# Performance work log

Measured on AMD Instinct MI355X. Metric: run time of the kernel, lower is better.

## Reference

```python
import jax, jax.numpy as jnp
import numpy as np

D_MODEL = 1024
N_HEADS = 16
HEAD_DIM = D_MODEL // N_HEADS
B, S = 4, 2048


def setup_inputs() -> dict:
    key = jax.random.key(0)
    ks = jax.random.split(key, 11)
    scale = 1.0 / np.sqrt(D_MODEL)
    inp = {
        "query": jax.random.normal(ks[0], (B, S, D_MODEL), jnp.float32),
        "key": jax.random.normal(ks[1], (B, S, D_MODEL), jnp.float32),
        "value": jax.random.normal(ks[2], (B, S, D_MODEL), jnp.float32),
        "Wq": jax.random.normal(ks[3], (D_MODEL, D_MODEL), jnp.float32) * scale,
        "bq": jnp.zeros((D_MODEL,), jnp.float32),
        "Wk": jax.random.normal(ks[4], (D_MODEL, D_MODEL), jnp.float32) * scale,
        "bk": jnp.zeros((D_MODEL,), jnp.float32),
        "Wv": jax.random.normal(ks[5], (D_MODEL, D_MODEL), jnp.float32) * scale,
        "bv": jnp.zeros((D_MODEL,), jnp.float32),
        "Wo": jax.random.normal(ks[6], (D_MODEL, D_MODEL), jnp.float32) * scale,
        "bo": jnp.zeros((D_MODEL,), jnp.float32),
    }
    return inp


def _split_heads(x):
    b, s, _ = x.shape
    return x.reshape(b, s, N_HEADS, HEAD_DIM).transpose(0, 2, 1, 3)  # b h s d


def reference(query, key, value, Wq, bq, Wk, bk, Wv, bv, Wo, bo):
    Q = _split_heads(query @ Wq.T + bq)
    K = _split_heads(key @ Wk.T + bk)
    V = _split_heads(value @ Wv.T + bv)
    scale = 1.0 / jnp.sqrt(jnp.float32(HEAD_DIM))
    energy = jnp.einsum("bhqd,bhkd->bhqk", Q, K) * scale  # full N x N scores
    attn = jax.nn.softmax(energy, axis=-1)
    x = jnp.einsum("bhqk,bhkd->bhqd", attn, V)
    x = x.transpose(0, 2, 1, 3).reshape(query.shape[0], -1, D_MODEL)
    return x @ Wo.T + bo
```

## Files before the change

kernel.cpp:

```cpp
#include <hip/hip_runtime.h>
#include <cstdint>
#include <cstddef>


typedef unsigned short u16;
typedef unsigned u32;
typedef short short8 __attribute__((ext_vector_type(8)));
typedef __bf16 bf16x8 __attribute__((ext_vector_type(8)));
typedef float f32x4 __attribute__((ext_vector_type(4)));
typedef float f32x16 __attribute__((ext_vector_type(16)));
typedef unsigned short u16x4 __attribute__((ext_vector_type(4)));
typedef unsigned u32x2 __attribute__((ext_vector_type(2)));
typedef unsigned u32x4 __attribute__((ext_vector_type(4)));
typedef int iv2 __attribute__((ext_vector_type(2)));

__device__ __forceinline__ u16 f2bf(float f) {
  unsigned u = __builtin_bit_cast(unsigned, f);
  u += 0x7fffu + ((u >> 16) & 1u);
  return (u16)(u >> 16);
}
__device__ __forceinline__ bf16x8 bc8(short8 v) { return __builtin_bit_cast(bf16x8, v); }
__device__ __forceinline__ u32 pk_bf16(float a, float b) {
  u32 r;
  asm("v_cvt_pk_bf16_f32 %0, %1, %2" : "=v"(r) : "v"(a), "v"(b));
  return r;
}
__device__ __forceinline__ void gload16(const u16* g, u16* l) {
  __builtin_amdgcn_global_load_lds((const __attribute__((address_space(1))) void*)g,
                                   (__attribute__((address_space(3))) void*)l, 16, 0, 0);
}

__global__ __launch_bounds__(256) void cvt_all(const float* __restrict__ q,
                                               const float* __restrict__ k,
                                               const float* __restrict__ v,
                                               const float* __restrict__ wq,
                                               const float* __restrict__ wk,
                                               const float* __restrict__ wv,
                                               const float* __restrict__ wo,
                                               u16* __restrict__ xq, u16* __restrict__ xk,
                                               u16* __restrict__ xv, u16* __restrict__ wqb,
                                               u16* __restrict__ wkb, u16* __restrict__ wvb,
                                               u16* __restrict__ wob) {
  const size_t i4 = (size_t)blockIdx.x * 256 + threadIdx.x;
  const size_t A4 = 1ull << 21, W4 = 1ull << 18;
  const float* s;
  u16* d;
  size_t off;
  if (i4 < 3 * A4) {
    const int r = (int)(i4 >> 21);
    off = i4 & (A4 - 1);
    s = r == 0 ? q : (r == 1 ? k : v);
    d = r == 0 ? xq : (r == 1 ? xk : xv);
  } else {
    const size_t t = i4 - 3 * A4;
    const int r = (int)(t >> 18);
    off = t & (W4 - 1);
    s = r == 0 ? wq : (r == 1 ? wk : (r == 2 ? wv : wo));
    d = r == 0 ? wqb : (r == 1 ? wkb : (r == 2 ? wvb : wob));
  }
  const f32x4 a = ((const f32x4*)s)[off];
  u32x2 o = {pk_bf16(a[0], a[1]), pk_bf16(a[2], a[3])};
  ((u32x2*)d)[off] = o;
}

__device__ __forceinline__ bf16x8 ldf(const u16* buf, int row, int g) {
  return bc8(*(const short8*)(buf + row * 32 + g * 8));
}

__device__ __forceinline__ void gemm_core(u16* lds, const u16* __restrict__ A,
                                          const u16* __restrict__ Bw,
                                          const float* __restrict__ bias,
                                          void* __restrict__ C, int mode, float oscale) {
  const int t = threadIdx.x;
  const int w = t >> 6, l = t & 63, g = l >> 4, m = l & 15;
  const int wr = w >> 1, wc = w & 1;
  const int m0 = blockIdx.x * 128, n0 = blockIdx.y * 256;
  const u16* gA = A + (size_t)m0 * 1024;
  const u16* gB = Bw + (size_t)n0 * 1024;

  f32x4 acc[4][8];
  const f32x4 z = {0.f, 0.f, 0.f, 0.f};
#pragma unroll
  for (int i = 0; i < 4; ++i)
#pragma unroll
    for (int j = 0; j < 8; ++j) acc[i][j] = z;

#pragma unroll
  for (int tt = 0; tt < 2; ++tt) {
    u16* sA = lds + tt * 12288;
    u16* sB = sA + 4096;
    const int ko = tt * 32;
#pragma unroll
    for (int r = 0; r < 2; ++r) {
      const int c = r * 256 + t;
      gload16(gA + (size_t)(c >> 2) * 1024 + (c & 3) * 8 + ko, sA + c * 8);
    }
#pragma unroll
    for (int r = 0; r < 4; ++r) {
      const int c = r * 256 + t;
      gload16(gB + (size_t)(c >> 2) * 1024 + (c & 3) * 8 + ko, sB + c * 8);
    }
  }
  asm volatile("s_waitcnt vmcnt(6)" ::: "memory");
  __builtin_amdgcn_s_barrier();

  bf16x8 af[4], bfr[8];
  int cb = 0;
  for (int tt = 0; tt < 32; ++tt) {
    u16* bA = lds + cb * 12288;
    u16* bB = bA + 4096;
    const int sbi = (cb == 0) ? 2 : cb - 1;
    u16* sA = lds + sbi * 12288;
    u16* sB = sA + 4096;
    const int ko = (tt + 2) * 32;
    const bool st = tt < 30;

    af[0] = ldf(bA, wr * 64 + m, g);
    af[1] = ldf(bA, wr * 64 + 16 + m, g);
#pragma unroll
    for (int j = 0; j < 4; ++j) bfr[j] = ldf(bB, wc * 128 + j * 16 + m, g);
    if (st) {
#pragma unroll
      for (int r = 0; r < 2; ++r) {
        const int c = r * 256 + t;
        gload16(gA + (size_t)(c >> 2) * 1024 + (c & 3) * 8 + ko, sA + c * 8);
      }
    }
    __builtin_amdgcn_s_barrier();
    __builtin_amdgcn_s_setprio(1);
#pragma unroll
    for (int i = 0; i < 2; ++i)
#pragma unroll
      for (int j = 0; j < 4; ++j)
        acc[i][j] = __builtin_amdgcn_mfma_f32_16x16x32_bf16(af[i], bfr[j], acc[i][j], 0, 0, 0);
    __builtin_amdgcn_s_setprio(0);
    __builtin_amdgcn_s_barrier();

#pragma unroll
    for (int j = 4; j < 8; ++j) bfr[j] = ldf(bB, wc * 128 + j * 16 + m, g);
    if (st) {
#pragma unroll
      for (int r = 0; r < 2; ++r) {
        const int c = r * 256 + t;
        gload16(gB + (size_t)(c >> 2) * 1024 + (c & 3) * 8 + ko, sB + c * 8);
      }
    }
    __builtin_amdgcn_s_barrier();
    __builtin_amdgcn_s_setprio(1);
#pragma unroll
    for (int i = 0; i < 2; ++i)
#pragma unroll
      for (int j = 4; j < 8; ++j)
        acc[i][j] = __builtin_amdgcn_mfma_f32_16x16x32_bf16(af[i], bfr[j], acc[i][j], 0, 0, 0);
    __builtin_amdgcn_s_setprio(0);
    __builtin_amdgcn_s_barrier();

    af[2] = ldf(bA, wr * 64 + 32 + m, g);
    af[3] = ldf(bA, wr * 64 + 48 + m, g);
    if (st) {
#pragma unroll
      for (int r = 2; r < 4; ++r) {
        const int c = r * 256 + t;
        gload16(gB + (size_t)(c >> 2) * 1024 + (c & 3) * 8 + ko, sB + c * 8);
      }
    }
    __builtin_amdgcn_s_barrier();
    __builtin_amdgcn_s_setprio(1);
#pragma unroll
    for (int i = 2; i < 4; ++i)
#pragma unroll
      for (int j = 0; j < 4; ++j)
        acc[i][j] = __builtin_amdgcn_mfma_f32_16x16x32_bf16(af[i], bfr[j], acc[i][j], 0, 0, 0);
    __builtin_amdgcn_s_setprio(0);
    __builtin_amdgcn_s_barrier();

    __builtin_amdgcn_s_setprio(1);
#pragma unroll
    for (int i = 2; i < 4; ++i)
#pragma unroll
      for (int j = 4; j < 8; ++j)
        acc[i][j] = __builtin_amdgcn_mfma_f32_16x16x32_bf16(af[i], bfr[j], acc[i][j], 0, 0, 0);
    __builtin_amdgcn_s_setprio(0);
    if (tt < 30)
      asm volatile("s_waitcnt vmcnt(6)" ::: "memory");
    else
      asm volatile("s_waitcnt vmcnt(0)" ::: "memory");
    __builtin_amdgcn_s_barrier();
    cb = (cb == 2) ? 0 : cb + 1;
  }

  float bv[8];
#pragma unroll
  for (int j = 0; j < 8; ++j) bv[j] = bias[n0 + wc * 128 + j * 16 + m];

  if (mode == 2) {
#pragma unroll
    for (int i = 0; i < 4; ++i)
#pragma unroll
      for (int j = 0; j < 8; ++j) {
        const int row0 = m0 + wr * 64 + i * 16 + g * 4;
        const int col = n0 + wc * 128 + j * 16 + m;
        u16x4 o;
#pragma unroll
        for (int r = 0; r < 4; ++r) o[r] = f2bf((acc[i][j][r] + bv[j]) * oscale);
        *(u16x4*)((u16*)C + ((size_t)(row0 >> 11) * 1024 + col) * 2048 + (row0 & 2047)) = o;
      }
  } else {
#pragma unroll
    for (int i = 0; i < 4; ++i) {
#pragma unroll
      for (int r = 0; r < 4; ++r) {
        const int row = m0 + wr * 64 + i * 16 + g * 4 + r;
#pragma unroll
        for (int j = 0; j < 8; ++j) {
          const int col = n0 + wc * 128 + j * 16 + m;
          const float v = (acc[i][j][r] + bv[j]) * oscale;
          if (mode == 0)
            ((float*)C)[(size_t)row * 1024 + col] = v;
          else
            ((u16*)C)[(size_t)row * 1024 + col] = f2bf(v);
        }
      }
    }
  }
}

__global__ __launch_bounds__(256, 2) void qkv_gemm(const u16* __restrict__ xq,
                                                   const u16* __restrict__ xk,
                                                   const u16* __restrict__ xv,
                                                   const u16* __restrict__ wqb,
                                                   const u16* __restrict__ wkb,
                                                   const u16* __restrict__ wvb,
                                                   const float* __restrict__ bq,
                                                   const float* __restrict__ bk,
                                                   const float* __restrict__ bv,
                                                   u16* __restrict__ Qp, u16* __restrict__ Kp,
                                                   u16* __restrict__ Vt, float SC) {
  __shared__ alignas(16) u16 lds[36864];
  const int z = blockIdx.z;
  const u16* A = z == 0 ? xq : (z == 1 ? xk : xv);
  const u16* W = z == 0 ? wqb : (z == 1 ? wkb : wvb);
  const float* bi = z == 0 ? bq : (z == 1 ? bk : bv);
  void* C = z == 0 ? (void*)Qp : (z == 1 ? (void*)Kp : (void*)Vt);
  gemm_core(lds, A, W, bi, C, z == 2 ? 2 : 1, z == 0 ? SC : 1.f);
}

__global__ __launch_bounds__(256, 2) void o_gemm(const u16* __restrict__ Xa,
                                                 const u16* __restrict__ wob,
                                                 const float* __restrict__ bo,
                                                 float* __restrict__ out) {
  __shared__ alignas(16) u16 lds[36864];
  gemm_core(lds, Xa, wob, bo, out, 0, 1.f);
}

__global__ __launch_bounds__(512, 4) void attn_fwd(const u16* __restrict__ Q,
                                                   const u16* __restrict__ Kp,
                                                   const u16* __restrict__ Vt,
                                                   u16* __restrict__ Xa) {
  __shared__ alignas(16) u16 kl[64][72];
  __shared__ alignas(16) u16 vl[64][72];
  const int tid = threadIdx.x;
  const int l = tid & 63, w = tid >> 6;
  const int q32 = l & 31, hi = l >> 5;
  const int lin = blockIdx.x + 8 * blockIdx.y;
  const int xp = lin >> 6, yp = lin & 63;
  const int b = yp >> 4, h = yp & 15;
  const int q0 = xp * 256 + w * 32;

  bf16x8 qf[4];
  const size_t qrow = (size_t)b * 2048 + q0 + q32;
#pragma unroll
  for (int ds = 0; ds < 4; ++ds)
    qf[ds] = bc8(*(const short8*)(Q + qrow * 1024 + h * 64 + ds * 16 + hi * 8));

  f32x16 of[2] = {{}, {}};
  float l0 = 0.f, l1 = 0.f, l2 = 0.f, l3 = 0.f;

  const int sr = tid >> 3;
  const int sc8 = (tid & 7) * 8;
  const u16* Kb = Kp + (size_t)b * 2048 * 1024 + h * 64;
  const u16* Vb = Vt + (size_t)yp * 64 * 2048;

  short8 rk = *(const short8*)(Kb + (size_t)sr * 1024 + sc8);
  short8 rv = *(const short8*)(Vb + (size_t)sr * 2048 + sc8);

  for (int kt = 0; kt < 32; ++kt) {
    *(short8*)(&kl[sr][sc8]) = rk;
    *(short8*)(&vl[sr][sc8]) = rv;
    __syncthreads();
    if (kt + 1 < 32) {
      rk = *(const short8*)(Kb + (size_t)((kt + 1) * 64 + sr) * 1024 + sc8);
      rv = *(const short8*)(Vb + (size_t)sr * 2048 + (kt + 1) * 64 + sc8);
    }

#pragma unroll
    for (int kt2 = 0; kt2 < 2; ++kt2) {
      f32x16 st = {};
#pragma unroll
      for (int ds = 0; ds < 4; ++ds) {
        const bf16x8 kf = bc8(*(const short8*)(&kl[kt2 * 32 + q32][ds * 16 + hi * 8]));
        st = __builtin_amdgcn_mfma_f32_32x32x16_bf16(kf, qf[ds], st, 0, 0, 0);
      }
      float p[16];
#pragma unroll
      for (int r = 0; r < 16; ++r) p[r] = __builtin_amdgcn_exp2f(st[r]);
      l0 += (p[0] + p[1]) + (p[2] + p[3]);
      l1 += (p[4] + p[5]) + (p[6] + p[7]);
      l2 += (p[8] + p[9]) + (p[10] + p[11]);
      l3 += (p[12] + p[13]) + (p[14] + p[15]);
#pragma unroll
      for (int s = 0; s < 2; ++s) {
        int X0 = (int)pk_bf16(p[8 * s + 0], p[8 * s + 1]);
        int X1 = (int)pk_bf16(p[8 * s + 2], p[8 * s + 3]);
        int Y0 = (int)pk_bf16(p[8 * s + 4], p[8 * s + 5]);
        int Y1 = (int)pk_bf16(p[8 * s + 6], p[8 * s + 7]);
        iv2 r0 = __builtin_amdgcn_permlane32_swap(X0, Y0, false, false);
        iv2 r1 = __builtin_amdgcn_permlane32_swap(X1, Y1, false, false);
        u32x4 bw = {(u32)r0[0], (u32)r1[0], (u32)r0[1], (u32)r1[1]};
        const bf16x8 pb = __builtin_bit_cast(bf16x8, bw);
        const int ks = kt2 * 2 + s;
#pragma unroll
        for (int dt = 0; dt < 2; ++dt) {
          const bf16x8 vf = bc8(*(const short8*)(&vl[dt * 32 + q32][ks * 16 + hi * 8]));
          of[dt] = __builtin_amdgcn_mfma_f32_32x32x16_bf16(vf, pb, of[dt], 0, 0, 0);
        }
      }
    }
    __syncthreads();
  }

  float lo = (l0 + l1) + (l2 + l3);
  lo += __shfl_xor(lo, 32, 64);
  const float inv = 1.0f / lo;

#pragma unroll
  for (int dt = 0; dt < 2; ++dt)
#pragma unroll
    for (int rg = 0; rg < 4; ++rg) {
      u32x2 o2;
      o2[0] = pk_bf16(of[dt][4 * rg + 0] * inv, of[dt][4 * rg + 1] * inv);
      o2[1] = pk_bf16(of[dt][4 * rg + 2] * inv, of[dt][4 * rg + 3] * inv);
      *(u32x2*)(Xa + qrow * 1024 + h * 64 + dt * 32 + rg * 8 + hi * 4) = o2;
    }
}

extern "C" void kernel_launch(void* const* d_in, const int* in_sizes, int n_in,
                              void* d_out, int out_size, void* d_ws, size_t ws_size,
                              hipStream_t stream) {
  const float* q  = (const float*)d_in[0];
  const float* k  = (const float*)d_in[1];
  const float* v  = (const float*)d_in[2];
  const float* Wq = (const float*)d_in[3];
  const float* bq = (const float*)d_in[4];
  const float* Wk = (const float*)d_in[5];
  const float* bk = (const float*)d_in[6];
  const float* Wv = (const float*)d_in[7];
  const float* bv = (const float*)d_in[8];
  const float* Wo = (const float*)d_in[9];
  const float* bo = (const float*)d_in[10];

  char* ws = (char*)d_ws;
  const size_t MB = 1024ull * 1024ull;
  u16* wqb = (u16*)(ws + 0 * MB);
  u16* wkb = (u16*)(ws + 2 * MB);
  u16* wvb = (u16*)(ws + 4 * MB);
  u16* wob = (u16*)(ws + 6 * MB);
  u16* xq  = (u16*)(ws + 8 * MB);
  u16* xk  = (u16*)(ws + 24 * MB);
  u16* xv  = (u16*)(ws + 40 * MB);
  u16* Qp  = (u16*)(ws + 56 * MB);
  u16* Kp  = (u16*)(ws + 72 * MB);
  u16* Vt  = (u16*)(ws + 88 * MB);
  u16* Xa  = xq;

  cvt_all<<<28672, 256, 0, stream>>>(q, k, v, Wq, Wk, Wv, Wo,
                                     xq, xk, xv, wqb, wkb, wvb, wob);

  const float SC = 0.125f * 1.44269504f;
  qkv_gemm<<<dim3(64, 4, 3), 256, 0, stream>>>(xq, xk, xv, wqb, wkb, wvb,
                                               bq, bk, bv, Qp, Kp, Vt, SC);

  attn_fwd<<<dim3(8, 64), 512, 0, stream>>>(Qp, Kp, Vt, Xa);

  o_gemm<<<dim3(64, 4), 256, 0, stream>>>(Xa, wob, bo, (float*)d_out);
}
```

Measured before the change: 192.4 us.

## Double-buffer K/V tiles in LDS and raise wave priority around MFMAs

The attention kernel now keeps two LDS buffers for the K and V tiles and drops one of the two barriers per iteration. While the current tile is consumed, the next tile is stored to the other buffer and the global loads run two tiles ahead. The QK^T MFMAs are all issued before the softmax exp work, and s_setprio raises wave priority around the MFMA blocks to help interleave waves. This doubles LDS use for K/V per block, which could affect occupancy at 4 blocks per CU, and adds register pressure from holding two score tiles.

Measured after the change: 193.2 us. No clear change (+0.4%).

```diff
diff --git a/kernel.cpp b/kernel.cpp
--- a/kernel.cpp
+++ b/kernel.cpp
@@ -257,8 +257,8 @@
                                                    const u16* __restrict__ Kp,
                                                    const u16* __restrict__ Vt,
                                                    u16* __restrict__ Xa) {
-  __shared__ alignas(16) u16 kl[64][72];
-  __shared__ alignas(16) u16 vl[64][72];
+  __shared__ alignas(16) u16 kl[2][64][72];
+  __shared__ alignas(16) u16 vl[2][64][72];
   const int tid = threadIdx.x;
   const int l = tid & 63, w = tid >> 6;
   const int q32 = l & 31, hi = l >> 5;
@@ -283,27 +283,43 @@
 
   short8 rk = *(const short8*)(Kb + (size_t)sr * 1024 + sc8);
   short8 rv = *(const short8*)(Vb + (size_t)sr * 2048 + sc8);
+  *(short8*)(&kl[0][sr][sc8]) = rk;
+  *(short8*)(&vl[0][sr][sc8]) = rv;
+  rk = *(const short8*)(Kb + (size_t)(64 + sr) * 1024 + sc8);
+  rv = *(const short8*)(Vb + (size_t)sr * 2048 + 64 + sc8);
+  __syncthreads();
 
   for (int kt = 0; kt < 32; ++kt) {
-    *(short8*)(&kl[sr][sc8]) = rk;
-    *(short8*)(&vl[sr][sc8]) = rv;
-    __syncthreads();
-    if (kt + 1 < 32) {
-      rk = *(const short8*)(Kb + (size_t)((kt + 1) * 64 + sr) * 1024 + sc8);
-      rv = *(const short8*)(Vb + (size_t)sr * 2048 + (kt + 1) * 64 + sc8);
-    }
-
+    const int cur = kt & 1;
+
+    f32x16 st2[2];
+    __builtin_amdgcn_s_setprio(1);
 #pragma unroll
     for (int kt2 = 0; kt2 < 2; ++kt2) {
       f32x16 st = {};
 #pragma unroll
       for (int ds = 0; ds < 4; ++ds) {
-        const bf16x8 kf = bc8(*(const short8*)(&kl[kt2 * 32 + q32][ds * 16 + hi * 8]));
+        const bf16x8 kf = bc8(*(const short8*)(&kl[cur][kt2 * 32 + q32][ds * 16 + hi * 8]));
         st = __builtin_amdgcn_mfma_f32_32x32x16_bf16(kf, qf[ds], st, 0, 0, 0);
       }
+      st2[kt2] = st;
+    }
+    __builtin_amdgcn_s_setprio(0);
+
+    if (kt + 1 < 32) {
+      *(short8*)(&kl[cur ^ 1][sr][sc8]) = rk;
+      *(short8*)(&vl[cur ^ 1][sr][sc8]) = rv;
+    }
+    if (kt + 2 < 32) {
+      rk = *(const short8*)(Kb + (size_t)((kt + 2) * 64 + sr) * 1024 + sc8);
+      rv = *(const short8*)(Vb + (size_t)sr * 2048 + (kt + 2) * 64 + sc8);
+    }
+
+#pragma unroll
+    for (int kt2 = 0; kt2 < 2; ++kt2) {
       float p[16];
 #pragma unroll
-      for (int r = 0; r < 16; ++r) p[r] = __builtin_amdgcn_exp2f(st[r]);
+      for (int r = 0; r < 16; ++r) p[r] = __builtin_amdgcn_exp2f(st2[kt2][r]);
       l0 += (p[0] + p[1]) + (p[2] + p[3]);
       l1 += (p[4] + p[5]) + (p[6] + p[7]);
       l2 += (p[8] + p[9]) + (p[10] + p[11]);
@@ -319,11 +335,13 @@
         u32x4 bw = {(u32)r0[0], (u32)r1[0], (u32)r0[1], (u32)r1[1]};
         const bf16x8 pb = __builtin_bit_cast(bf16x8, bw);
         const int ks = kt2 * 2 + s;
+        __builtin_amdgcn_s_setprio(1);
 #pragma unroll
         for (int dt = 0; dt < 2; ++dt) {
-          const bf16x8 vf = bc8(*(const short8*)(&vl[dt * 32 + q32][ks * 16 + hi * 8]));
+          const bf16x8 vf = bc8(*(const short8*)(&vl[cur][dt * 32 + q32][ks * 16 + hi * 8]));
           of[dt] = __builtin_amdgcn_mfma_f32_32x32x16_bf16(vf, pb, of[dt], 0, 0, 0);
         }
+        __builtin_amdgcn_s_setprio(0);
       }
     }
     __syncthreads();
```
